# Kernel tuning notes

Measured on AMD Instinct MI355X. Metric: run time of the kernel, lower is better.

Reference implementation:

```python
import jax, jax.numpy as jnp
import numpy as np

T, B, IN, H = 512, 4096, 1, 12

def setup_inputs() -> dict:
    key = jax.random.key(0)
    ks = jax.random.split(key, 7)
    s = 1.0 / np.sqrt(H)
    return {
        "X": jax.random.normal(ks[0], (T, B, IN), dtype=jnp.float32),
        "W_ih": jax.random.uniform(ks[1], (4 * H, IN), minval=-s, maxval=s, dtype=jnp.float32),
        "W_hh": jax.random.uniform(ks[2], (4 * H, H), minval=-s, maxval=s, dtype=jnp.float32),
        "b_ih": jax.random.uniform(ks[3], (4 * H,), minval=-s, maxval=s, dtype=jnp.float32),
        "b_hh": jax.random.uniform(ks[4], (4 * H,), minval=-s, maxval=s, dtype=jnp.float32),
        "fc_w": jax.random.uniform(ks[5], (1, H), minval=-s, maxval=s, dtype=jnp.float32),
        "fc_b": jax.random.uniform(ks[6], (1,), minval=-s, maxval=s, dtype=jnp.float32),
    }

def reference(X, W_ih, W_hh, b_ih, b_hh, fc_w, fc_b):
    # Precompute input contribution for all timesteps: [T, B, 4H]
    x_proj = jnp.einsum('tbi,gi->tbg', X, W_ih) + b_ih + b_hh
    h0 = jnp.zeros((X.shape[1], H), dtype=X.dtype)
    c0 = jnp.zeros_like(h0)

    def step(carry, xp_t):
        h, c = carry
        gates = xp_t + h @ W_hh.T  # [B, 4H]
        i, f, g, o = jnp.split(gates, 4, axis=-1)  # PyTorch gate order i,f,g,o
        i = jax.nn.sigmoid(i)
        f = jax.nn.sigmoid(f)
        g = jnp.tanh(g)
        o = jax.nn.sigmoid(o)
        c_new = f * c + i * g
        h_new = o * jnp.tanh(c_new)
        return (h_new, c_new), h_new

    _, hs = jax.lax.scan(step, (h0, c0), x_proj)  # hs: [T, B, H]
    return jnp.einsum('tbh,oh->tbo', hs, fc_w) + fc_b  # [T, B, 1]
```

## Files before the change

### kernel.cpp

```cpp
#include <hip/hip_runtime.h>


#define TT    512
#define NB    4096
#define HH    12
#define RPW   4
#define CHUNK 64

typedef float v2f __attribute__((ext_vector_type(2)));

static __device__ __forceinline__ v2f pkfma(v2f a, v2f b, v2f c) {
#if __has_builtin(__builtin_elementwise_fma)
    return __builtin_elementwise_fma(a, b, c);
#else
    v2f r; r.x = fmaf(a.x, b.x, c.x); r.y = fmaf(a.y, b.y, c.y); return r;
#endif
}

#define SNEG (-1.44269504088896340736f)
#define SPOS ( 2.88539008177792681472f)

#define ROR(r) (0x120 + (r))

__global__ __launch_bounds__(64, 1)
void lstm_fused(const float* __restrict__ X,
                const float* __restrict__ W_ih,
                const float* __restrict__ W_hh,
                const float* __restrict__ b_ih,
                const float* __restrict__ b_hh,
                const float* __restrict__ fc_w,
                const float* __restrict__ fc_b,
                float* __restrict__ out)
{
    __shared__ float xchunk[CHUNK][RPW];

    const int lane = threadIdx.x;
    const int row  = lane >> 4;
    const int j    = lane & 15;
    const int cellbase = blockIdx.x * RPW;
    const int cell = cellbase + row;

    int sid[16];
    sid[0] = j;
#define PROBE(r) sid[r] = __builtin_amdgcn_update_dpp(0, j, ROR(r), 0xF, 0xF, true);
    PROBE(1)  PROBE(2)  PROBE(3)  PROBE(4)  PROBE(5)
    PROBE(6)  PROBE(7)  PROBE(8)  PROBE(9)  PROBE(10)
    PROBE(11) PROBE(12) PROBE(13) PROBE(14) PROBE(15)
#undef PROBE

    const int jc = (j < HH) ? j : (HH - 1);
    v2f   wifU[16], wgoU[16];
    float fcwU[16];
    #pragma unroll
    for (int r = 0; r < 16; ++r) {
        const int  s  = sid[r];
        const int  sc = (s < HH) ? s : (HH - 1);
        const float g = ((j >= HH) || (s < HH)) ? 1.0f : 0.0f;
        wifU[r].x = g * SNEG * W_hh[(0 * HH + jc) * HH + sc];
        wifU[r].y = g * SNEG * W_hh[(1 * HH + jc) * HH + sc];
        wgoU[r].x = g * SPOS * W_hh[(2 * HH + jc) * HH + sc];
        wgoU[r].y = g * SNEG * W_hh[(3 * HH + jc) * HH + sc];
        fcwU[r]   = g * fc_w[sc];
    }
    v2f bif, bgo, wxif, wxgo;
    bif.x  = SNEG * (b_ih[0 * HH + jc] + b_hh[0 * HH + jc]);
    bif.y  = SNEG * (b_ih[1 * HH + jc] + b_hh[1 * HH + jc]);
    bgo.x  = SPOS * (b_ih[2 * HH + jc] + b_hh[2 * HH + jc]);
    bgo.y  = SNEG * (b_ih[3 * HH + jc] + b_hh[3 * HH + jc]);
    wxif.x = SNEG * W_ih[0 * HH + jc];
    wxif.y = SNEG * W_ih[1 * HH + jc];
    wxgo.x = SPOS * W_ih[2 * HH + jc];
    wxgo.y = SNEG * W_ih[3 * HH + jc];
    const float fcb = fc_b[0];

    float cst = 0.0f;
    float hn  = 0.0f;
    int hbits = 0;

    for (int t = 0; t < TT; ++t) {
        if ((t & (CHUNK - 1)) == 0) {
            const float4 q = *(const float4*)(X + (size_t)(t + lane) * NB + cellbase);
            *(float4*)&xchunk[lane][0] = q;
        }
        const float xv = xchunk[t & (CHUNK - 1)][row];

        v2f gifA = bif, goA = bgo;
        v2f gifB; gifB.x = 0.0f; gifB.y = 0.0f;
        v2f goB;  goB.x  = 0.0f; goB.y  = 0.0f;
        float fco = fcb;
        {
            v2f hk; hk.x = hn; hk.y = hn;
            gifA = pkfma(wifU[0], hk, gifA);
            goA  = pkfma(wgoU[0], hk, goA);
            fco  = fmaf(hn, fcwU[0], fco);
        }
#define XR(r) { \
        const int   hr_##r = __builtin_amdgcn_update_dpp(0, hbits, ROR(r), 0xF, 0xF, true); \
        const float hf = __int_as_float(hr_##r); \
        v2f hk; hk.x = hf; hk.y = hf; \
        if ((r) < 8) { gifA = pkfma(wifU[r], hk, gifA); goA = pkfma(wgoU[r], hk, goA); } \
        else         { gifB = pkfma(wifU[r], hk, gifB); goB = pkfma(wgoU[r], hk, goB); } \
        fco = fmaf(hf, fcwU[r], fco); }
        XR(1)  XR(2)  XR(3)  XR(4)  XR(5)
        XR(6)  XR(7)  XR(8)  XR(9)  XR(10)
        XR(11) XR(12) XR(13) XR(14) XR(15)

        if (t > 0 && j == 0) out[(size_t)(t - 1) * NB + cell] = fco;

        v2f gif = gifA + gifB;
        v2f ggo = goA + goB;
        v2f xvv; xvv.x = xv; xvv.y = xv;
        gif = pkfma(xvv, wxif, gif);
        ggo = pkfma(xvv, wxgo, ggo);

        const float si = __builtin_amdgcn_rcpf(1.0f + __builtin_amdgcn_exp2f(gif.x));
        const float sf = __builtin_amdgcn_rcpf(1.0f + __builtin_amdgcn_exp2f(gif.y));
        const float rg = __builtin_amdgcn_rcpf(1.0f + __builtin_amdgcn_exp2f(ggo.x));
        const float so = __builtin_amdgcn_rcpf(1.0f + __builtin_amdgcn_exp2f(ggo.y));
        const float tg = fmaf(-2.0f, rg, 1.0f);
        cst = fmaf(sf, cst, si * tg);
        const float rc   = __builtin_amdgcn_rcpf(1.0f + __builtin_amdgcn_exp2f(SPOS * cst));
        const float m2so = -2.0f * so;
        hn    = fmaf(m2so, rc, so);
        hbits = __float_as_int(hn);
    }

    {
        float fco = fmaf(hn, fcwU[0], fcb);
#define XF(r) { \
        const int hr_##r = __builtin_amdgcn_update_dpp(0, hbits, ROR(r), 0xF, 0xF, true); \
        fco = fmaf(__int_as_float(hr_##r), fcwU[r], fco); }
        XF(1)  XF(2)  XF(3)  XF(4)  XF(5)
        XF(6)  XF(7)  XF(8)  XF(9)  XF(10)
        XF(11) XF(12) XF(13) XF(14) XF(15)
        if (j == 0) out[(size_t)(TT - 1) * NB + cell] = fco;
    }
}

extern "C" void kernel_launch(void* const* d_in, const int* in_sizes, int n_in,
                              void* d_out, int out_size, void* d_ws, size_t ws_size,
                              hipStream_t stream) {
    const float* X    = (const float*)d_in[0];
    const float* W_ih = (const float*)d_in[1];
    const float* W_hh = (const float*)d_in[2];
    const float* b_ih = (const float*)d_in[3];
    const float* b_hh = (const float*)d_in[4];
    const float* fc_w = (const float*)d_in[5];
    const float* fc_b = (const float*)d_in[6];
    float* out = (float*)d_out;

    const int grid = NB / RPW;
    lstm_fused<<<grid, 64, 0, stream>>>(X, W_ih, W_hh, b_ih, b_hh, fc_w, fc_b, out);
}
```

Measured before the change: 204.9 us.

## Prefetch X chunks into registers, transpose LDS layout, use DPP tree for FC output

Loads the next 64-step X chunk into registers one chunk ahead so the global load latency is hidden behind compute. The shared buffer is transposed so each row reads four timesteps with a single float4 LDS load. The per-step FC projection drops its 16-term FMA chain in favour of a 4-step DPP rotate-add reduction after h is computed, which removes the fcw register array. This adds a small serial DPP chain to each step and shifts where the output store happens.

```diff
diff --git a/kernel.cpp b/kernel.cpp
--- a/kernel.cpp
+++ b/kernel.cpp
@@ -32,7 +32,7 @@
                 const float* __restrict__ fc_b,
                 float* __restrict__ out)
 {
-    __shared__ float xchunk[CHUNK][RPW];
+    __shared__ float xchunk[RPW][CHUNK];
 
     const int lane = threadIdx.x;
     const int row  = lane >> 4;
@@ -49,8 +49,7 @@
 #undef PROBE
 
     const int jc = (j < HH) ? j : (HH - 1);
-    v2f   wifU[16], wgoU[16];
-    float fcwU[16];
+    v2f wifU[16], wgoU[16];
     #pragma unroll
     for (int r = 0; r < 16; ++r) {
         const int  s  = sid[r];
@@ -60,7 +59,6 @@
         wifU[r].y = g * SNEG * W_hh[(1 * HH + jc) * HH + sc];
         wgoU[r].x = g * SPOS * W_hh[(2 * HH + jc) * HH + sc];
         wgoU[r].y = g * SNEG * W_hh[(3 * HH + jc) * HH + sc];
-        fcwU[r]   = g * fc_w[sc];
     }
     v2f bif, bgo, wxif, wxgo;
     bif.x  = SNEG * (b_ih[0 * HH + jc] + b_hh[0 * HH + jc]);
@@ -71,69 +69,72 @@
     wxif.y = SNEG * W_ih[1 * HH + jc];
     wxgo.x = SPOS * W_ih[2 * HH + jc];
     wxgo.y = SNEG * W_ih[3 * HH + jc];
-    const float fcb = fc_b[0];
+    const float fcb  = fc_b[0];
+    const float fcwj = (j < HH) ? fc_w[j] : 0.0f;
 
     float cst = 0.0f;
     float hn  = 0.0f;
     int hbits = 0;
 
-    for (int t = 0; t < TT; ++t) {
-        if ((t & (CHUNK - 1)) == 0) {
-            const float4 q = *(const float4*)(X + (size_t)(t + lane) * NB + cellbase);
-            *(float4*)&xchunk[lane][0] = q;
+    float4 gq = *(const float4*)(X + (size_t)lane * NB + cellbase);
+
+    for (int tc = 0; tc < TT; tc += CHUNK) {
+        xchunk[0][lane] = gq.x;
+        xchunk[1][lane] = gq.y;
+        xchunk[2][lane] = gq.z;
+        xchunk[3][lane] = gq.w;
+        if (tc + CHUNK < TT)
+            gq = *(const float4*)(X + (size_t)(tc + CHUNK + lane) * NB + cellbase);
+
+        for (int t4 = 0; t4 < CHUNK; t4 += 4) {
+            const float4 xq = *(const float4*)&xchunk[row][t4];
+            const float xs[4] = {xq.x, xq.y, xq.z, xq.w};
+
+            #pragma unroll
+            for (int u = 0; u < 4; ++u) {
+                v2f gifA = bif, goA = bgo;
+                v2f gifB; gifB.x = 0.0f; gifB.y = 0.0f;
+                v2f goB;  goB.x  = 0.0f; goB.y  = 0.0f;
+                {
+                    v2f hk; hk.x = hn; hk.y = hn;
+                    gifA = pkfma(wifU[0], hk, gifA);
+                    goA  = pkfma(wgoU[0], hk, goA);
+                }
+#define XR(r) { \
+                const int hr_##r = __builtin_amdgcn_update_dpp(0, hbits, ROR(r), 0xF, 0xF, true); \
+                const float hf = __int_as_float(hr_##r); \
+                v2f hk; hk.x = hf; hk.y = hf; \
+                if ((r) < 8) { gifA = pkfma(wifU[r], hk, gifA); goA = pkfma(wgoU[r], hk, goA); } \
+                else         { gifB = pkfma(wifU[r], hk, gifB); goB = pkfma(wgoU[r], hk, goB); } }
+                XR(1)  XR(2)  XR(3)  XR(4)  XR(5)
+                XR(6)  XR(7)  XR(8)  XR(9)  XR(10)
+                XR(11) XR(12) XR(13) XR(14) XR(15)
+#undef XR
+                v2f gif = gifA + gifB;
+                v2f ggo = goA + goB;
+                v2f xvv; xvv.x = xs[u]; xvv.y = xs[u];
+                gif = pkfma(xvv, wxif, gif);
+                ggo = pkfma(xvv, wxgo, ggo);
+
+                const float si = __builtin_amdgcn_rcpf(1.0f + __builtin_amdgcn_exp2f(gif.x));
+                const float sf = __builtin_amdgcn_rcpf(1.0f + __builtin_amdgcn_exp2f(gif.y));
+                const float rg = __builtin_amdgcn_rcpf(1.0f + __builtin_amdgcn_exp2f(ggo.x));
+                const float so = __builtin_amdgcn_rcpf(1.0f + __builtin_amdgcn_exp2f(ggo.y));
+                const float tg = fmaf(-2.0f, rg, 1.0f);
+                cst = fmaf(sf, cst, si * tg);
+                const float rc   = __builtin_amdgcn_rcpf(1.0f + __builtin_amdgcn_exp2f(SPOS * cst));
+                const float m2so = -2.0f * so;
+                hn    = fmaf(m2so, rc, so);
+                hbits = __float_as_int(hn);
+
+                float p = hn * fcwj;
+                p += __int_as_float(__builtin_amdgcn_update_dpp(0, __float_as_int(p), ROR(8), 0xF, 0xF, true));
+                p += __int_as_float(__builtin_amdgcn_update_dpp(0, __float_as_int(p), ROR(4), 0xF, 0xF, true));
+                p += __int_as_float(__builtin_amdgcn_update_dpp(0, __float_as_int(p), ROR(2), 0xF, 0xF, true));
+                p += __int_as_float(__builtin_amdgcn_update_dpp(0, __float_as_int(p), ROR(1), 0xF, 0xF, true));
+                if (j == 0) out[(size_t)(tc + t4 + u) * NB + cell] = p + fcb;
+            }
         }
-        const float xv = xchunk[t & (CHUNK - 1)][row];
-
-        v2f gifA = bif, goA = bgo;
-        v2f gifB; gifB.x = 0.0f; gifB.y = 0.0f;
-        v2f goB;  goB.x  = 0.0f; goB.y  = 0.0f;
-        float fco = fcb;
-        {
-            v2f hk; hk.x = hn; hk.y = hn;
-            gifA = pkfma(wifU[0], hk, gifA);
-            goA  = pkfma(wgoU[0], hk, goA);
-            fco  = fmaf(hn, fcwU[0], fco);
-        }
-#define XR(r) { \
-        const int   hr_##r = __builtin_amdgcn_update_dpp(0, hbits, ROR(r), 0xF, 0xF, true); \
-        const float hf = __int_as_float(hr_##r); \
-        v2f hk; hk.x = hf; hk.y = hf; \
-        if ((r) < 8) { gifA = pkfma(wifU[r], hk, gifA); goA = pkfma(wgoU[r], hk, goA); } \
-        else         { gifB = pkfma(wifU[r], hk, gifB); goB = pkfma(wgoU[r], hk, goB); } \
-        fco = fmaf(hf, fcwU[r], fco); }
-        XR(1)  XR(2)  XR(3)  XR(4)  XR(5)
-        XR(6)  XR(7)  XR(8)  XR(9)  XR(10)
-        XR(11) XR(12) XR(13) XR(14) XR(15)
-
-        if (t > 0 && j == 0) out[(size_t)(t - 1) * NB + cell] = fco;
-
-        v2f gif = gifA + gifB;
-        v2f ggo = goA + goB;
-        v2f xvv; xvv.x = xv; xvv.y = xv;
-        gif = pkfma(xvv, wxif, gif);
-        ggo = pkfma(xvv, wxgo, ggo);
-
-        const float si = __builtin_amdgcn_rcpf(1.0f + __builtin_amdgcn_exp2f(gif.x));
-        const float sf = __builtin_amdgcn_rcpf(1.0f + __builtin_amdgcn_exp2f(gif.y));
-        const float rg = __builtin_amdgcn_rcpf(1.0f + __builtin_amdgcn_exp2f(ggo.x));
-        const float so = __builtin_amdgcn_rcpf(1.0f + __builtin_amdgcn_exp2f(ggo.y));
-        const float tg = fmaf(-2.0f, rg, 1.0f);
-        cst = fmaf(sf, cst, si * tg);
-        const float rc   = __builtin_amdgcn_rcpf(1.0f + __builtin_amdgcn_exp2f(SPOS * cst));
-        const float m2so = -2.0f * so;
-        hn    = fmaf(m2so, rc, so);
-        hbits = __float_as_int(hn);
-    }
-
-    {
-        float fco = fmaf(hn, fcwU[0], fcb);
-#define XF(r) { \
-        const int hr_##r = __builtin_amdgcn_update_dpp(0, hbits, ROR(r), 0xF, 0xF, true); \
-        fco = fmaf(__int_as_float(hr_##r), fcwU[r], fco); }
-        XF(1)  XF(2)  XF(3)  XF(4)  XF(5)
-        XF(6)  XF(7)  XF(8)  XF(9)  XF(10)
-        XF(11) XF(12) XF(13) XF(14) XF(15)
-        if (j == 0) out[(size_t)(TT - 1) * NB + cell] = fco;
     }
 }
 
```

Measured after the change: 184.0 us. 1.11x faster.
